# Optimization experiments

Measured on AMD Instinct MI355X. Metric: run time of the kernel, lower is better.

The kernel has to match this reference:

```python
import jax, jax.numpy as jnp
import numpy as np

NFFT = 1024
HOP = 512
N_FREQ = NFFT // 2
B = 16
T = 4096


def _istft_kernels(nfft):
    # Same construction as _get_istft_kernels in the torch source.
    t = np.arange(nfft, dtype=np.float64)[:, None]
    f = np.arange(nfft // 2 + 1, dtype=np.float64)[None, :]
    k = np.exp(1j * (2.0 * np.pi * t * f) / nfft)  # [nfft, nfft/2+1]
    ac_cof = float(np.real(k[0, 0]))  # == 1.0
    k = 2.0 * k[:, 1:]
    k[:, -1] = k[:, -1] / 2.0
    return (np.real(k).astype(np.float32),  # [nfft, n_freq]
            np.imag(k).astype(np.float32),
            ac_cof)


def setup_inputs() -> dict:
    key = jax.random.key(0)
    k1, k2, k3 = jax.random.split(key, 3)
    magn = jax.random.normal(k1, (B, 1, N_FREQ, T), dtype=jnp.float32)
    phase = jax.random.normal(k2, (B, 1, N_FREQ, T), dtype=jnp.float32)
    ac = jax.random.normal(k3, (B, 1, T), dtype=jnp.float32)
    rk, ik, _ = _istft_kernels(NFFT)
    return {
        "magn": magn,
        "phase": phase,
        "ac": ac,
        "real_kernels": jnp.asarray(rk),   # [nfft, n_freq]
        "imag_kernels": jnp.asarray(ik),   # [nfft, n_freq]
    }


def reference(magn, phase, ac, real_kernels, imag_kernels):
    nfft, hop = NFFT, HOP
    ac_cof = 1.0  # real(exp(0)) from kernels[0, 0]
    real_part = jnp.einsum('bft,of->bot', magn[:, 0], real_kernels)   # [B, nfft, T]
    imag_part = jnp.einsum('bft,of->bot', -phase[:, 0], imag_kernels)  # [B, nfft, T]
    frames = (real_part - imag_part + ac_cof * ac) / float(nfft)       # ac [B,1,T] broadcasts
    # conv_transpose2d with identity kernel [nfft,1,1,nfft], stride=hop == overlap-add
    b, _, t = frames.shape
    out_len = (t - 1) * hop + nfft
    idx = jnp.arange(t)[:, None] * hop + jnp.arange(nfft)[None, :]     # [T, nfft]
    sig = jnp.zeros((b, out_len), frames.dtype)
    sig = sig.at[:, idx].add(jnp.swapaxes(frames, 1, 2))               # scatter-add frames
    return sig
```

## Files before the change

### kernel.cpp

```cpp
#include <hip/hip_runtime.h>
#include <hip/hip_bf16.h>

typedef __bf16 bf16;
typedef __bf16 bf16x4 __attribute__((ext_vector_type(4)));
typedef __bf16 bf16x8 __attribute__((ext_vector_type(8)));
typedef float  f32x4  __attribute__((ext_vector_type(4)));

#define T_SZ   4096
#define NFREQ  512
#define HOP    512
#define OUT_LEN 2097664
#define NTT33  33
#define XROWS  4097

#define XW_ELEMS ((size_t)16 * XROWS * 1024)
#define WT_ELEMS ((size_t)512 * 1024)
#define WS_NEED  ((XW_ELEMS + WT_ELEMS) * 2)

__device__ __forceinline__ void gl16(const void* g, void* l) {
    __builtin_amdgcn_global_load_lds(
        (const __attribute__((address_space(1))) void*)g,
        (__attribute__((address_space(3))) void*)l, 16, 0, 0);
}


__global__ __launch_bounds__(256, 4) void cvt_w(const float* __restrict__ rk,
                                                const float* __restrict__ ik,
                                                bf16* __restrict__ Wt) {
    const int j  = blockIdx.x;
    const int k4 = threadIdx.x * 4;
    const float* s = (k4 < NFREQ) ? &rk[j * NFREQ + k4] : &ik[j * NFREQ + k4 - NFREQ];
    f32x4 v = *(const f32x4*)s;
    bf16x4 h;
    h[0] = (bf16)v[0]; h[1] = (bf16)v[1]; h[2] = (bf16)v[2]; h[3] = (bf16)v[3];
    *(bf16x4*)&Wt[((size_t)j << 10) + k4] = h;
}

__global__ __launch_bounds__(256, 4) void cvt_x(const float* __restrict__ magn,
                                                const float* __restrict__ phase,
                                                bf16* __restrict__ Xw) {
    __shared__ float t2[64][133];
    const int tid = threadIdx.x;
    const int bid = blockIdx.x;
    const int kt  = bid & 15;
    const int tt  = (bid >> 4) & 31;
    const int b   = bid >> 9;
    const float* srcb = (kt < 8 ? magn : phase)
                      + ((size_t)b * NFREQ + (kt & 7) * 64) * T_SZ + tt * 128;
    const int fr = tid >> 5;
    const int cc = (tid & 31) * 4;
    #pragma unroll
    for (int p = 0; p < 8; ++p) {
        const int f = fr + 8 * p;
        f32x4 v = *(const f32x4*)&srcb[(size_t)f * T_SZ + cc];
        t2[f][cc + 0] = v[0]; t2[f][cc + 1] = v[1];
        t2[f][cc + 2] = v[2]; t2[f][cc + 3] = v[3];
    }
    if (tid < 64)
        t2[tid][128] = (tt > 0) ? srcb[(size_t)tid * T_SZ - 1] : 0.f;
    __syncthreads();

    const int koff = (tid & 7) * 8;
    bf16* dstb = Xw + (((size_t)b * XROWS + tt * 128) << 10) + kt * 64 + koff;
    #pragma unroll
    for (int q = 0; q < 4; ++q) {
        const int tr  = (tid >> 3) + 32 * q;
        const int im1 = tr ? (tr - 1) : 128;
        bf16x8 o;
        #pragma unroll
        for (int ki = 0; ki < 8; ++ki) {
            const int f = koff + ki;
            const float sgn = (f & 1) ? 1.f : -1.f;
            o[ki] = (bf16)(t2[f][tr] + sgn * t2[f][im1]);
        }
        *(bf16x8*)&dstb[(size_t)tr << 10] = o;
    }
    if (tt == 31 && tid < 8) {
        bf16x8 o;
        #pragma unroll
        for (int ki = 0; ki < 8; ++ki) {
            const int f = tid * 8 + ki;
            const float sgn = (f & 1) ? 1.f : -1.f;
            o[ki] = (bf16)(sgn * t2[f][127]);
        }
        *(bf16x8*)&Xw[(((size_t)b * XROWS + 4096) << 10) + kt * 64 + tid * 8] = o;
    }
}

__global__ __launch_bounds__(256, 4) void istft_gemmY4(
    const bf16* __restrict__ Xw, const bf16* __restrict__ Wt,
    const float* __restrict__ acv, float* __restrict__ out)
{
    __shared__ __attribute__((aligned(16))) bf16 As[2][128 * 32];
    __shared__ __attribute__((aligned(16))) bf16 Bs[2][128 * 32];

    const int tid = threadIdx.x;
    const int w   = tid >> 6;
    const int l   = tid & 63;
    const int wr  = w >> 1, wc = w & 1;
    const int c15 = l & 15, c4 = l >> 4;

    const int bid = blockIdx.x;
    const int xcd = bid & 7;
    const int idx = bid >> 3;
    const int jt  = idx & 3;
    const int png = idx >> 2;
    const int pnl = png * 8 + xcd;
    const int b   = pnl / NTT33;
    const int tt0 = pnl - b * NTT33;
    const int j0  = jt * 128;
    const int t0  = tt0 * 128;
    const size_t xb = (size_t)b * XROWS;

    const int ssrc = ((l & 3) ^ ((l >> 2) & 3) ^ ((l >> 4) & 3)) * 8;
    const int srow = 16 * w + (l >> 2);

    const size_t asrc0 = ((size_t)(j0 + srow)) << 10;
    const size_t asrc1 = ((size_t)(j0 + 64 + srow)) << 10;
    int tq0 = t0 + srow;        if (tq0 > 4096) tq0 = 4096;
    int tq1 = t0 + 64 + srow;   if (tq1 > 4096) tq1 = 4096;
    const size_t bsrc0 = (xb + tq0) << 10;
    const size_t bsrc1 = (xb + tq1) << 10;

    auto stage = [&](int p, int ks) {
        const int k0 = ks * 32;
        gl16(Wt + asrc0 + k0 + ssrc, &As[p][(16 * w) * 32]);
        gl16(Wt + asrc1 + k0 + ssrc, &As[p][(64 + 16 * w) * 32]);
        gl16(Xw + bsrc0 + k0 + ssrc, &Bs[p][(16 * w) * 32]);
        gl16(Xw + bsrc1 + k0 + ssrc, &Bs[p][(64 + 16 * w) * 32]);
    };

    const float* acb = acv + (size_t)b * T_SZ;
    float acs_r[4];
    #pragma unroll
    for (int n = 0; n < 4; ++n) {
        const int tt = t0 + wc * 64 + n * 16 + c15;
        const float a0 = (tt < T_SZ) ? acb[tt] : 0.f;
        const float a1 = (tt >= 1 && tt <= T_SZ) ? acb[tt - 1] : 0.f;
        acs_r[n] = a0 + a1;
    }

    f32x4 acc[4][4];
    #pragma unroll
    for (int i = 0; i < 4; ++i)
        #pragma unroll
        for (int j = 0; j < 4; ++j)
            acc[i][j] = (f32x4){0.f, 0.f, 0.f, 0.f};

    bf16x8 a[4], bb[4];
    auto rdFrags = [&](int p) {
        #pragma unroll
        for (int m = 0; m < 4; ++m) {
            const int r = wr * 64 + m * 16 + c15;
            const int s = ((c4 ^ r ^ (r >> 2)) & 3) * 8;
            a[m] = *(const bf16x8*)&As[p][r * 32 + s];
        }
        #pragma unroll
        for (int n = 0; n < 4; ++n) {
            const int r = wc * 64 + n * 16 + c15;
            const int s = ((c4 ^ r ^ (r >> 2)) & 3) * 8;
            bb[n] = *(const bf16x8*)&Bs[p][r * 32 + s];
        }
    };

    stage(0, 0);
    __syncthreads();

    for (int ks = 0; ks < 32; ++ks) {
        const int P = ks & 1;
        if (ks + 1 < 32) stage(P ^ 1, ks + 1);
        rdFrags(P);
        #pragma unroll
        for (int m = 0; m < 4; ++m)
            #pragma unroll
            for (int n = 0; n < 4; ++n)
                acc[m][n] = __builtin_amdgcn_mfma_f32_16x16x32_bf16(
                    a[m], bb[n], acc[m][n], 0, 0, 0);
        __syncthreads();
    }

    const float inv = 1.0f / 1024.0f;
    float* ob = out + (size_t)b * OUT_LEN;
    const int jbase = j0 + wr * 64 + c4 * 4;
    #pragma unroll
    for (int n = 0; n < 4; ++n) {
        const int tt = t0 + wc * 64 + n * 16 + c15;
        if (tt <= 4096) {
            #pragma unroll
            for (int m = 0; m < 4; ++m) {
                f32x4 v;
                #pragma unroll
                for (int rr = 0; rr < 4; ++rr)
                    v[rr] = (acc[m][n][rr] + acs_r[n]) * inv;
                __builtin_nontemporal_store(v, (f32x4*)&ob[(size_t)tt * HOP + jbase + m * 16]);
            }
        }
    }
}

#define LDBL 40
__global__ __launch_bounds__(256, 2) void istft_fused_legacy(
    const float* __restrict__ magn, const float* __restrict__ phase,
    const float* __restrict__ acv,
    const float* __restrict__ rk,  const float* __restrict__ ik,
    float* __restrict__ out)
{
    __shared__ __attribute__((aligned(16))) bf16 As[2][128 * LDBL];
    __shared__ __attribute__((aligned(16))) bf16 Bs[2][129 * LDBL];
    const int tid = threadIdx.x;
    const int w = tid >> 6, l = tid & 63;
    const int bid = blockIdx.x;
    const int xcd = bid & 7, q = bid >> 3;
    const int jt = q & 7, pgrp = q >> 3;
    const int pnl = pgrp * 8 + xcd;
    const int b = pnl / NTT33, tt0 = pnl - b * NTT33;
    const int j0 = jt * 64, t0 = tt0 * 128;
    const float* xm = magn  + (size_t)b * NFREQ * T_SZ;
    const float* xp = phase + (size_t)b * NFREQ * T_SZ;
    const int jrow = tid >> 3, fc = (tid & 7) * 4;
    const int f0 = (tid >> 5) * 4, tl = tid & 31;
    f32x4 areg[4]; float vreg[4][4]; float rz = 0.f;
    f32x4 acc[8][2];
    #pragma unroll
    for (int i = 0; i < 8; ++i)
        #pragma unroll
        for (int j = 0; j < 2; ++j) acc[i][j] = (f32x4){0.f, 0.f, 0.f, 0.f};
    const int nbase = w * 32;
    auto loadA = [&](int ks) {
        const int k0 = ks * 32;
        const float* wsrc = (k0 < NFREQ) ? (rk + k0) : (ik + (k0 - NFREQ));
        #pragma unroll
        for (int i = 0; i < 4; ++i) {
            const int jr = jrow + 32 * i;
            const int j = (jr < 64) ? (j0 + jr) : (j0 + 448 + jr);
            areg[i] = *(const f32x4*)&wsrc[(size_t)j * NFREQ + fc];
        }
    };
    auto writeA = [&](int p) {
        #pragma unroll
        for (int i = 0; i < 4; ++i) {
            bf16x4 v;
            v[0] = (bf16)areg[i][0]; v[1] = (bf16)areg[i][1];
            v[2] = (bf16)areg[i][2]; v[3] = (bf16)areg[i][3];
            *(bf16x4*)&As[p][(jrow + 32 * i) * LDBL + fc] = v;
        }
    };
    auto loadB = [&](int ks) {
        const int k0 = ks * 32;
        const float* xbp = (k0 < NFREQ) ? (xm + (size_t)k0 * T_SZ)
                                        : (xp + (size_t)(k0 - NFREQ) * T_SZ);
        #pragma unroll
        for (int i = 0; i < 4; ++i) {
            if (t0 + 32 * i + 32 <= T_SZ) {
                #pragma unroll
                for (int fj = 0; fj < 4; ++fj)
                    vreg[fj][i] = xbp[(size_t)(f0 + fj) * T_SZ + t0 + tl + 32 * i];
            } else {
                #pragma unroll
                for (int fj = 0; fj < 4; ++fj) vreg[fj][i] = 0.f;
            }
        }
        if (tid < 32) rz = (t0 >= 1) ? xbp[(size_t)tid * T_SZ + (t0 - 1)] : 0.f;
    };
    auto writeB = [&](int p) {
        #pragma unroll
        for (int i = 0; i < 4; ++i) {
            bf16x4 v;
            v[0] = (bf16)vreg[0][i]; v[1] = (bf16)vreg[1][i];
            v[2] = (bf16)vreg[2][i]; v[3] = (bf16)vreg[3][i];
            *(bf16x4*)&Bs[p][(1 + tl + 32 * i) * LDBL + f0] = v;
        }
        if (tid < 32) Bs[p][tid] = (bf16)rz;
    };
    loadA(0); loadB(0); writeA(0); writeB(0);
    __syncthreads();
    int p = 0;
    for (int ks = 0; ks < 32; ++ks) {
        if (ks + 1 < 32) { loadA(ks + 1); loadB(ks + 1); }
        bf16x8 af[8], blv[2], bhv[2];
        #pragma unroll
        for (int mi = 0; mi < 8; ++mi)
            af[mi] = *(const bf16x8*)&As[p][(mi * 16 + (l & 15)) * LDBL + (l >> 4) * 8];
        #pragma unroll
        for (int ni = 0; ni < 2; ++ni) {
            const int rb = nbase + ni * 16 + (l & 15);
            bhv[ni] = *(const bf16x8*)&Bs[p][rb * LDBL + (l >> 4) * 8];
            blv[ni] = *(const bf16x8*)&Bs[p][(rb + 1) * LDBL + (l >> 4) * 8];
        }
        #pragma unroll
        for (int ni = 0; ni < 2; ++ni)
            #pragma unroll
            for (int mi = 0; mi < 4; ++mi) {
                acc[mi][ni] = __builtin_amdgcn_mfma_f32_16x16x32_bf16(af[mi], blv[ni], acc[mi][ni], 0, 0, 0);
                acc[mi + 4][ni] = __builtin_amdgcn_mfma_f32_16x16x32_bf16(af[mi + 4], bhv[ni], acc[mi + 4][ni], 0, 0, 0);
            }
        if (ks + 1 < 32) { writeA(p ^ 1); writeB(p ^ 1); }
        __syncthreads();
        p ^= 1;
    }
    const float inv = 1.0f / 1024.0f;
    float* ob = out + (size_t)b * OUT_LEN;
    const float* acb = acv + (size_t)b * T_SZ;
    #pragma unroll
    for (int ni = 0; ni < 2; ++ni) {
        const int tt = t0 + nbase + ni * 16 + (l & 15);
        if (tt <= T_SZ) {
            float acs = 0.f;
            if (tt < T_SZ) acs += acb[tt];
            if (tt >= 1)   acs += acb[tt - 1];
            #pragma unroll
            for (int mi = 0; mi < 4; ++mi) {
                const int jl = j0 + mi * 16 + (l >> 4) * 4;
                f32x4 v;
                #pragma unroll
                for (int rr = 0; rr < 4; ++rr)
                    v[rr] = (acc[mi][ni][rr] + acc[mi + 4][ni][rr] + acs) * inv;
                __builtin_nontemporal_store(v, (f32x4*)&ob[(size_t)tt * HOP + jl]);
            }
        }
    }
}

extern "C" void kernel_launch(void* const* d_in, const int* in_sizes, int n_in,
                              void* d_out, int out_size, void* d_ws, size_t ws_size,
                              hipStream_t stream) {
    const float* magn  = (const float*)d_in[0];
    const float* phase = (const float*)d_in[1];
    const float* ac    = (const float*)d_in[2];
    const float* rk    = (const float*)d_in[3];
    const float* ik    = (const float*)d_in[4];
    float* out = (float*)d_out;

    if (ws_size >= WS_NEED) {
        bf16* Xw = (bf16*)d_ws;
        bf16* Wt = Xw + XW_ELEMS;
        cvt_w<<<512, 256, 0, stream>>>(rk, ik, Wt);
        cvt_x<<<8192, 256, 0, stream>>>(magn, phase, Xw);
        istft_gemmY4<<<2112, 256, 0, stream>>>(Xw, Wt, ac, out);
    } else {
        istft_fused_legacy<<<528 * 8, 256, 0, stream>>>(magn, phase, ac, rk, ik, out);
    }
}
```

Before: 181.1 us.

## Merge conversion kernels, deepen GEMM K-tile, peel tail row into dot-product epilogue

Folds the weight conversion into the activation conversion kernel, so one launch does both and a kernel boundary disappears. The GEMM K-step grows from 32 to 64 using a new XOR swizzle, which halves the number of barrier iterations. The grid is reduced from 33 to 32 time tiles per batch, and the final overlap row (t=4096) is now computed by a scalar dot-product epilogue in the last tile. In exchange, LDS use doubles and the launch bound drops to 2 blocks per CU, which lowers occupancy. The scalar tail adds serial work on a few blocks.

After: 218.1 us. 20.4% more time.

```diff
diff --git a/kernel.cpp b/kernel.cpp
--- a/kernel.cpp
+++ b/kernel.cpp
@@ -24,24 +24,27 @@
 }
 
 
-__global__ __launch_bounds__(256, 4) void cvt_w(const float* __restrict__ rk,
-                                                const float* __restrict__ ik,
-                                                bf16* __restrict__ Wt) {
-    const int j  = blockIdx.x;
-    const int k4 = threadIdx.x * 4;
-    const float* s = (k4 < NFREQ) ? &rk[j * NFREQ + k4] : &ik[j * NFREQ + k4 - NFREQ];
-    f32x4 v = *(const f32x4*)s;
-    bf16x4 h;
-    h[0] = (bf16)v[0]; h[1] = (bf16)v[1]; h[2] = (bf16)v[2]; h[3] = (bf16)v[3];
-    *(bf16x4*)&Wt[((size_t)j << 10) + k4] = h;
-}
-
-__global__ __launch_bounds__(256, 4) void cvt_x(const float* __restrict__ magn,
-                                                const float* __restrict__ phase,
-                                                bf16* __restrict__ Xw) {
+__global__ __launch_bounds__(256, 4) void cvt_all(const float* __restrict__ magn,
+                                                  const float* __restrict__ phase,
+                                                  const float* __restrict__ rk,
+                                                  const float* __restrict__ ik,
+                                                  bf16* __restrict__ Wt,
+                                                  bf16* __restrict__ Xw) {
     __shared__ float t2[64][133];
     const int tid = threadIdx.x;
     const int bid = blockIdx.x;
+
+    if (bid >= 8192) {
+        const int j  = bid - 8192;
+        const int k4 = tid * 4;
+        const float* s = (k4 < NFREQ) ? &rk[j * NFREQ + k4] : &ik[j * NFREQ + k4 - NFREQ];
+        f32x4 v = *(const f32x4*)s;
+        bf16x4 h;
+        h[0] = (bf16)v[0]; h[1] = (bf16)v[1]; h[2] = (bf16)v[2]; h[3] = (bf16)v[3];
+        *(bf16x4*)&Wt[((size_t)j << 10) + k4] = h;
+        return;
+    }
+
     const int kt  = bid & 15;
     const int tt  = (bid >> 4) & 31;
     const int b   = bid >> 9;
@@ -87,12 +90,12 @@
     }
 }
 
-__global__ __launch_bounds__(256, 4) void istft_gemmY4(
+__global__ __launch_bounds__(256, 2) void istft_gemmY6(
     const bf16* __restrict__ Xw, const bf16* __restrict__ Wt,
     const float* __restrict__ acv, float* __restrict__ out)
 {
-    __shared__ __attribute__((aligned(16))) bf16 As[2][128 * 32];
-    __shared__ __attribute__((aligned(16))) bf16 Bs[2][128 * 32];
+    __shared__ __attribute__((aligned(16))) bf16 As[2][128 * 64];
+    __shared__ __attribute__((aligned(16))) bf16 Bs[2][128 * 64];
 
     const int tid = threadIdx.x;
     const int w   = tid >> 6;
@@ -102,32 +105,33 @@
 
     const int bid = blockIdx.x;
     const int xcd = bid & 7;
-    const int idx = bid >> 3;
-    const int jt  = idx & 3;
-    const int png = idx >> 2;
-    const int pnl = png * 8 + xcd;
-    const int b   = pnl / NTT33;
-    const int tt0 = pnl - b * NTT33;
+    const int jt  = (bid >> 3) & 3;
+    const int pg  = bid >> 5;
+    const int pnl = pg * 8 + xcd;
+    const int b   = pnl >> 5;
+    const int tt0 = pnl & 31;
     const int j0  = jt * 128;
     const int t0  = tt0 * 128;
     const size_t xb = (size_t)b * XROWS;
 
-    const int ssrc = ((l & 3) ^ ((l >> 2) & 3) ^ ((l >> 4) & 3)) * 8;
-    const int srow = 16 * w + (l >> 2);
-
-    const size_t asrc0 = ((size_t)(j0 + srow)) << 10;
-    const size_t asrc1 = ((size_t)(j0 + 64 + srow)) << 10;
-    int tq0 = t0 + srow;        if (tq0 > 4096) tq0 = 4096;
-    int tq1 = t0 + 64 + srow;   if (tq1 > 4096) tq1 = 4096;
-    const size_t bsrc0 = (xb + tq0) << 10;
-    const size_t bsrc1 = (xb + tq1) << 10;
+    const int sr8 = l >> 3;
+    const int ssk = ((l & 7) ^ sr8) * 8;
+    size_t asrc[4], bsrc[4];
+    #pragma unroll
+    for (int i = 0; i < 4; ++i) {
+        const int R = w * 8 + i * 32 + sr8;
+        asrc[i] = ((size_t)(j0 + R)) << 10;
+        bsrc[i] = (xb + t0 + R) << 10;
+    }
 
     auto stage = [&](int p, int ks) {
-        const int k0 = ks * 32;
-        gl16(Wt + asrc0 + k0 + ssrc, &As[p][(16 * w) * 32]);
-        gl16(Wt + asrc1 + k0 + ssrc, &As[p][(64 + 16 * w) * 32]);
-        gl16(Xw + bsrc0 + k0 + ssrc, &Bs[p][(16 * w) * 32]);
-        gl16(Xw + bsrc1 + k0 + ssrc, &Bs[p][(64 + 16 * w) * 32]);
+        const int k0 = ks * 64;
+        #pragma unroll
+        for (int i = 0; i < 4; ++i)
+            gl16(Wt + asrc[i] + k0 + ssk, &As[p][(w * 8 + i * 32) * 64]);
+        #pragma unroll
+        for (int i = 0; i < 4; ++i)
+            gl16(Xw + bsrc[i] + k0 + ssk, &Bs[p][(w * 8 + i * 32) * 64]);
     };
 
     const float* acb = acv + (size_t)b * T_SZ;
@@ -135,9 +139,7 @@
     #pragma unroll
     for (int n = 0; n < 4; ++n) {
         const int tt = t0 + wc * 64 + n * 16 + c15;
-        const float a0 = (tt < T_SZ) ? acb[tt] : 0.f;
-        const float a1 = (tt >= 1 && tt <= T_SZ) ? acb[tt - 1] : 0.f;
-        acs_r[n] = a0 + a1;
+        acs_r[n] = acb[tt] + (tt ? acb[tt - 1] : 0.f);
     }
 
     f32x4 acc[4][4];
@@ -148,28 +150,37 @@
             acc[i][j] = (f32x4){0.f, 0.f, 0.f, 0.f};
 
     bf16x8 a[4], bb[4];
-    auto rdFrags = [&](int p) {
+    auto rdA = [&](int p, int kk) {
         #pragma unroll
         for (int m = 0; m < 4; ++m) {
             const int r = wr * 64 + m * 16 + c15;
-            const int s = ((c4 ^ r ^ (r >> 2)) & 3) * 8;
-            a[m] = *(const bf16x8*)&As[p][r * 32 + s];
-        }
+            const int s = ((kk * 4 + c4) ^ (r & 7)) * 8;
+            a[m] = *(const bf16x8*)&As[p][r * 64 + s];
+        }
+    };
+    auto rdB = [&](int p, int kk) {
         #pragma unroll
         for (int n = 0; n < 4; ++n) {
             const int r = wc * 64 + n * 16 + c15;
-            const int s = ((c4 ^ r ^ (r >> 2)) & 3) * 8;
-            bb[n] = *(const bf16x8*)&Bs[p][r * 32 + s];
+            const int s = ((kk * 4 + c4) ^ (r & 7)) * 8;
+            bb[n] = *(const bf16x8*)&Bs[p][r * 64 + s];
         }
     };
 
     stage(0, 0);
     __syncthreads();
 
-    for (int ks = 0; ks < 32; ++ks) {
+    for (int ks = 0; ks < 16; ++ks) {
         const int P = ks & 1;
-        if (ks + 1 < 32) stage(P ^ 1, ks + 1);
-        rdFrags(P);
+        if (ks + 1 < 16) stage(P ^ 1, ks + 1);
+        rdA(P, 0); rdB(P, 0);
+        #pragma unroll
+        for (int m = 0; m < 4; ++m)
+            #pragma unroll
+            for (int n = 0; n < 4; ++n)
+                acc[m][n] = __builtin_amdgcn_mfma_f32_16x16x32_bf16(
+                    a[m], bb[n], acc[m][n], 0, 0, 0);
+        rdA(P, 1); rdB(P, 1);
         #pragma unroll
         for (int m = 0; m < 4; ++m)
             #pragma unroll
@@ -185,15 +196,34 @@
     #pragma unroll
     for (int n = 0; n < 4; ++n) {
         const int tt = t0 + wc * 64 + n * 16 + c15;
-        if (tt <= 4096) {
-            #pragma unroll
-            for (int m = 0; m < 4; ++m) {
-                f32x4 v;
+        #pragma unroll
+        for (int m = 0; m < 4; ++m) {
+            f32x4 v;
+            #pragma unroll
+            for (int rr = 0; rr < 4; ++rr)
+                v[rr] = (acc[m][n][rr] + acs_r[n]) * inv;
+            __builtin_nontemporal_store(v, (f32x4*)&ob[(size_t)tt * HOP + jbase + m * 16]);
+        }
+    }
+
+    if (tt0 == 31) {
+        __syncthreads();
+        if (tid < 128)
+            *(bf16x8*)&As[0][tid * 8] =
+                *(const bf16x8*)&Xw[((xb + 4096) << 10) + tid * 8];
+        __syncthreads();
+        if (tid < 128) {
+            const int j = j0 + tid;
+            const bf16* wrow = Wt + ((size_t)j << 10);
+            float s = 0.f;
+            for (int i = 0; i < 128; ++i) {
+                bf16x8 wv = *(const bf16x8*)&wrow[i * 8];
+                bf16x8 yv = *(const bf16x8*)&As[0][i * 8];
                 #pragma unroll
-                for (int rr = 0; rr < 4; ++rr)
-                    v[rr] = (acc[m][n][rr] + acs_r[n]) * inv;
-                __builtin_nontemporal_store(v, (f32x4*)&ob[(size_t)tt * HOP + jbase + m * 16]);
+                for (int e = 0; e < 8; ++e)
+                    s += (float)wv[e] * (float)yv[e];
             }
+            ob[(size_t)4096 * HOP + j] = (s + acb[4095]) * inv;
         }
     }
 }
@@ -334,9 +364,8 @@
     if (ws_size >= WS_NEED) {
         bf16* Xw = (bf16*)d_ws;
         bf16* Wt = Xw + XW_ELEMS;
-        cvt_w<<<512, 256, 0, stream>>>(rk, ik, Wt);
-        cvt_x<<<8192, 256, 0, stream>>>(magn, phase, Xw);
-        istft_gemmY4<<<2112, 256, 0, stream>>>(Xw, Wt, ac, out);
+        cvt_all<<<8704, 256, 0, stream>>>(magn, phase, rk, ik, Wt, Xw);
+        istft_gemmY6<<<2048, 256, 0, stream>>>(Xw, Wt, ac, out);
     } else {
         istft_fused_legacy<<<528 * 8, 256, 0, stream>>>(magn, phase, ac, rk, ik, out);
     }
```

## Enlarge GEMM tiles to 256x256 with 512 threads and merge conversion kernels

Applied to the files above, without the earlier changes.

The GEMM moves from 128x128 tiles on 256-thread blocks to 256x256 tiles on 512-thread blocks, with each wave holding 8x4 MFMA accumulators. This halves the global loads per output and lets the grid divide evenly over the time axis. The leftover boundary row (t=4096) is now handled by a scalar dot-product tail inside the last tile. The two bf16 conversion kernels are merged into one launch to save launch overhead. The larger tile raises register and LDS pressure, which may lower occupancy, and the scalar tail adds serial work to some blocks.

Measured after the change: 498.0 us. 2.75x slower.

```diff
diff --git a/kernel.cpp b/kernel.cpp
--- a/kernel.cpp
+++ b/kernel.cpp
@@ -24,24 +24,27 @@
 }
 
 
-__global__ __launch_bounds__(256, 4) void cvt_w(const float* __restrict__ rk,
-                                                const float* __restrict__ ik,
-                                                bf16* __restrict__ Wt) {
-    const int j  = blockIdx.x;
-    const int k4 = threadIdx.x * 4;
-    const float* s = (k4 < NFREQ) ? &rk[j * NFREQ + k4] : &ik[j * NFREQ + k4 - NFREQ];
-    f32x4 v = *(const f32x4*)s;
-    bf16x4 h;
-    h[0] = (bf16)v[0]; h[1] = (bf16)v[1]; h[2] = (bf16)v[2]; h[3] = (bf16)v[3];
-    *(bf16x4*)&Wt[((size_t)j << 10) + k4] = h;
-}
-
-__global__ __launch_bounds__(256, 4) void cvt_x(const float* __restrict__ magn,
-                                                const float* __restrict__ phase,
-                                                bf16* __restrict__ Xw) {
+__global__ __launch_bounds__(256, 4) void cvt_all(const float* __restrict__ magn,
+                                                  const float* __restrict__ phase,
+                                                  const float* __restrict__ rk,
+                                                  const float* __restrict__ ik,
+                                                  bf16* __restrict__ Wt,
+                                                  bf16* __restrict__ Xw) {
     __shared__ float t2[64][133];
     const int tid = threadIdx.x;
     const int bid = blockIdx.x;
+
+    if (bid >= 8192) {
+        const int j  = bid - 8192;
+        const int k4 = tid * 4;
+        const float* s = (k4 < NFREQ) ? &rk[j * NFREQ + k4] : &ik[j * NFREQ + k4 - NFREQ];
+        f32x4 v = *(const f32x4*)s;
+        bf16x4 h;
+        h[0] = (bf16)v[0]; h[1] = (bf16)v[1]; h[2] = (bf16)v[2]; h[3] = (bf16)v[3];
+        *(bf16x4*)&Wt[((size_t)j << 10) + k4] = h;
+        return;
+    }
+
     const int kt  = bid & 15;
     const int tt  = (bid >> 4) & 31;
     const int b   = bid >> 9;
@@ -87,47 +90,45 @@
     }
 }
 
-__global__ __launch_bounds__(256, 4) void istft_gemmY4(
+__global__ __launch_bounds__(512, 4) void istft_gemmY7(
     const bf16* __restrict__ Xw, const bf16* __restrict__ Wt,
     const float* __restrict__ acv, float* __restrict__ out)
 {
-    __shared__ __attribute__((aligned(16))) bf16 As[2][128 * 32];
-    __shared__ __attribute__((aligned(16))) bf16 Bs[2][128 * 32];
+    __shared__ __attribute__((aligned(16))) bf16 As[2][256 * 32];
+    __shared__ __attribute__((aligned(16))) bf16 Bs[2][256 * 32];
 
     const int tid = threadIdx.x;
     const int w   = tid >> 6;
     const int l   = tid & 63;
-    const int wr  = w >> 1, wc = w & 1;
+    const int wr  = w >> 2, wc = w & 3;
     const int c15 = l & 15, c4 = l >> 4;
 
     const int bid = blockIdx.x;
     const int xcd = bid & 7;
     const int idx = bid >> 3;
-    const int jt  = idx & 3;
-    const int png = idx >> 2;
+    const int jt  = idx & 1;
+    const int png = idx >> 1;
     const int pnl = png * 8 + xcd;
-    const int b   = pnl / NTT33;
-    const int tt0 = pnl - b * NTT33;
-    const int j0  = jt * 128;
-    const int t0  = tt0 * 128;
+    const int b   = pnl >> 4;
+    const int tt0 = pnl & 15;
+    const int j0  = jt * 256;
+    const int t0  = tt0 * 256;
     const size_t xb = (size_t)b * XROWS;
 
     const int ssrc = ((l & 3) ^ ((l >> 2) & 3) ^ ((l >> 4) & 3)) * 8;
     const int srow = 16 * w + (l >> 2);
 
     const size_t asrc0 = ((size_t)(j0 + srow)) << 10;
-    const size_t asrc1 = ((size_t)(j0 + 64 + srow)) << 10;
-    int tq0 = t0 + srow;        if (tq0 > 4096) tq0 = 4096;
-    int tq1 = t0 + 64 + srow;   if (tq1 > 4096) tq1 = 4096;
-    const size_t bsrc0 = (xb + tq0) << 10;
-    const size_t bsrc1 = (xb + tq1) << 10;
+    const size_t asrc1 = ((size_t)(j0 + 128 + srow)) << 10;
+    const size_t bsrc0 = (xb + t0 + srow) << 10;
+    const size_t bsrc1 = (xb + t0 + 128 + srow) << 10;
 
     auto stage = [&](int p, int ks) {
         const int k0 = ks * 32;
         gl16(Wt + asrc0 + k0 + ssrc, &As[p][(16 * w) * 32]);
-        gl16(Wt + asrc1 + k0 + ssrc, &As[p][(64 + 16 * w) * 32]);
+        gl16(Wt + asrc1 + k0 + ssrc, &As[p][(128 + 16 * w) * 32]);
         gl16(Xw + bsrc0 + k0 + ssrc, &Bs[p][(16 * w) * 32]);
-        gl16(Xw + bsrc1 + k0 + ssrc, &Bs[p][(64 + 16 * w) * 32]);
+        gl16(Xw + bsrc1 + k0 + ssrc, &Bs[p][(128 + 16 * w) * 32]);
     };
 
     const float* acb = acv + (size_t)b * T_SZ;
@@ -135,23 +136,21 @@
     #pragma unroll
     for (int n = 0; n < 4; ++n) {
         const int tt = t0 + wc * 64 + n * 16 + c15;
-        const float a0 = (tt < T_SZ) ? acb[tt] : 0.f;
-        const float a1 = (tt >= 1 && tt <= T_SZ) ? acb[tt - 1] : 0.f;
-        acs_r[n] = a0 + a1;
-    }
-
-    f32x4 acc[4][4];
-    #pragma unroll
-    for (int i = 0; i < 4; ++i)
+        acs_r[n] = acb[tt] + (tt ? acb[tt - 1] : 0.f);
+    }
+
+    f32x4 acc[8][4];
+    #pragma unroll
+    for (int i = 0; i < 8; ++i)
         #pragma unroll
         for (int j = 0; j < 4; ++j)
             acc[i][j] = (f32x4){0.f, 0.f, 0.f, 0.f};
 
-    bf16x8 a[4], bb[4];
+    bf16x8 a[8], bb[4];
     auto rdFrags = [&](int p) {
         #pragma unroll
-        for (int m = 0; m < 4; ++m) {
-            const int r = wr * 64 + m * 16 + c15;
+        for (int m = 0; m < 8; ++m) {
+            const int r = wr * 128 + m * 16 + c15;
             const int s = ((c4 ^ r ^ (r >> 2)) & 3) * 8;
             a[m] = *(const bf16x8*)&As[p][r * 32 + s];
         }
@@ -171,7 +170,7 @@
         if (ks + 1 < 32) stage(P ^ 1, ks + 1);
         rdFrags(P);
         #pragma unroll
-        for (int m = 0; m < 4; ++m)
+        for (int m = 0; m < 8; ++m)
             #pragma unroll
             for (int n = 0; n < 4; ++n)
                 acc[m][n] = __builtin_amdgcn_mfma_f32_16x16x32_bf16(
@@ -181,19 +180,38 @@
 
     const float inv = 1.0f / 1024.0f;
     float* ob = out + (size_t)b * OUT_LEN;
-    const int jbase = j0 + wr * 64 + c4 * 4;
+    const int jbase = j0 + wr * 128 + c4 * 4;
     #pragma unroll
     for (int n = 0; n < 4; ++n) {
         const int tt = t0 + wc * 64 + n * 16 + c15;
-        if (tt <= 4096) {
+        #pragma unroll
+        for (int m = 0; m < 8; ++m) {
+            f32x4 v;
             #pragma unroll
-            for (int m = 0; m < 4; ++m) {
-                f32x4 v;
+            for (int rr = 0; rr < 4; ++rr)
+                v[rr] = (acc[m][n][rr] + acs_r[n]) * inv;
+            __builtin_nontemporal_store(v, (f32x4*)&ob[(size_t)tt * HOP + jbase + m * 16]);
+        }
+    }
+
+    if (tt0 == 15) {
+        __syncthreads();
+        if (tid < 128)
+            *(bf16x8*)&As[0][tid * 8] =
+                *(const bf16x8*)&Xw[((xb + 4096) << 10) + tid * 8];
+        __syncthreads();
+        if (tid < 256) {
+            const int j = j0 + tid;
+            const bf16* wrow = Wt + ((size_t)j << 10);
+            float s = 0.f;
+            for (int i = 0; i < 128; ++i) {
+                bf16x8 wv = *(const bf16x8*)&wrow[i * 8];
+                bf16x8 yv = *(const bf16x8*)&As[0][i * 8];
                 #pragma unroll
-                for (int rr = 0; rr < 4; ++rr)
-                    v[rr] = (acc[m][n][rr] + acs_r[n]) * inv;
-                __builtin_nontemporal_store(v, (f32x4*)&ob[(size_t)tt * HOP + jbase + m * 16]);
+                for (int e = 0; e < 8; ++e)
+                    s += (float)wv[e] * (float)yv[e];
             }
+            ob[(size_t)4096 * HOP + j] = (s + acb[4095]) * inv;
         }
     }
 }
@@ -334,9 +352,8 @@
     if (ws_size >= WS_NEED) {
         bf16* Xw = (bf16*)d_ws;
         bf16* Wt = Xw + XW_ELEMS;
-        cvt_w<<<512, 256, 0, stream>>>(rk, ik, Wt);
-        cvt_x<<<8192, 256, 0, stream>>>(magn, phase, Xw);
-        istft_gemmY4<<<2112, 256, 0, stream>>>(Xw, Wt, ac, out);
+        cvt_all<<<8704, 256, 0, stream>>>(magn, phase, rk, ik, Wt, Xw);
+        istft_gemmY7<<<512, 512, 0, stream>>>(Xw, Wt, ac, out);
     } else {
         istft_fused_legacy<<<528 * 8, 256, 0, stream>>>(magn, phase, ac, rk, ik, out);
     }
```
